# Performance work log

Hardware: AMD Instinct MI355X
Metric: run time of the kernel (lower is better)

## Reference

```python
import jax, jax.numpy as jnp
import numpy as np

B, N, C, T = 64, 1000, 64, 32


def setup_inputs() -> dict:
    key = jax.random.key(0)
    k = jax.random.split(key, 6)
    scale = 0.05
    return {
        "X": jax.random.normal(k[0], (B, N, C, T), dtype=jnp.float32),
        "U1": jax.random.normal(k[1], (N,), dtype=jnp.float32) * scale,
        "U2": jax.random.normal(k[2], (C, N), dtype=jnp.float32) * scale,
        "U3": jax.random.normal(k[3], (C,), dtype=jnp.float32) * scale,
        "be": jax.random.normal(k[4], (T, T), dtype=jnp.float32) * scale,
        "Ve": jax.random.normal(k[5], (T, T), dtype=jnp.float32) * scale,
    }


def reference(X, U1, U2, U3, be, Ve):
    # lhs: (X^T(0,3,2,1) @ U1) @ U2  -> (B, T, N)
    lhs = jnp.einsum('bnct,n->btc', X, U1) @ U2          # (B,T,N)
    # rhs: (X^T(0,3,1,2) @ U3)^T      -> (B, N, T)
    rhs = jnp.einsum('bnct,c->bnt', X, U3)               # (B,N,T)
    # scores: (B,T,T) + be
    scores = jnp.einsum('btn,bns->bts', lhs, rhs) + be   # (B,T,T)
    E = jnp.einsum('ts,bsu->btu', Ve, jax.nn.sigmoid(scores))  # Ve @ sigmoid
    E = jax.nn.softmax(E, axis=1)                        # softmax over dim=1
    # X_hat = X @ E (broadcast over node dim): (B,N,C,T) @ (B,1,T,T)
    X_hat = jnp.einsum('bnct,bts->bncs', X, E)
    return X_hat
```

## Files before the change

### kernel.cpp

```cpp
#include <hip/hip_runtime.h>
#include <math.h>

#define BB 64
#define NN 1000
#define CC 64
#define TT 32
#define NCH 40
#define NCHUNKS 25

typedef float floatx4 __attribute__((ext_vector_type(4)));

__global__ __launch_bounds__(256) void k_p1(const float* __restrict__ X,
                                            const float* __restrict__ U1,
                                            const float* __restrict__ U3,
                                            float* __restrict__ rhs,
                                            float* __restrict__ Apart) {
    int b  = blockIdx.x / NCHUNKS;
    int ch = blockIdx.x % NCHUNKS;
    int t  = threadIdx.x & 31;
    int nl = threadIdx.x >> 5;
    int n0 = ch * NCH;

    float accA[CC];
#pragma unroll
    for (int c = 0; c < CC; ++c) accA[c] = 0.f;

    for (int i = 0; i < NCH / 8; ++i) {
        int n = n0 + i * 8 + nl;
        const float* xp = X + ((size_t)(b * NN + n) * CC) * TT + t;
        float u1 = U1[n];
        float r = 0.f;
#pragma unroll
        for (int c = 0; c < CC; ++c) {
            float x = __builtin_nontemporal_load(&xp[c * TT]);
            r += U3[c] * x;
            accA[c] += u1 * x;
        }
        rhs[(size_t)(b * NN + n) * TT + t] = r;
    }

    __shared__ float buf[8][32][9];
    int t2 = threadIdx.x & 31;
    int j2 = threadIdx.x >> 5;
    for (int strip = 0; strip < 8; ++strip) {
        __syncthreads();
#pragma unroll
        for (int j = 0; j < 8; ++j) buf[nl][t][j] = accA[strip * 8 + j];
        __syncthreads();
        float v = 0.f;
#pragma unroll
        for (int k = 0; k < 8; ++k) v += buf[k][t2][j2];
        Apart[((size_t)(ch * BB + b) * TT + t2) * CC + strip * 8 + j2] = v;
    }
}

__global__ __launch_bounds__(256) void k_G(const float* __restrict__ rhs,
                                           const float* __restrict__ U2,
                                           float* __restrict__ G) {
    size_t idx = (size_t)blockIdx.x * blockDim.x + threadIdx.x;
    int s = (int)(idx & 31);
    int c = (int)((idx >> 5) & (CC - 1));
    int b = (int)(idx >> 11);
    const float* rp = rhs + (size_t)b * NN * TT + s;
    const float* up = U2 + (size_t)c * NN;
    float a0 = 0.f, a1 = 0.f, a2 = 0.f, a3 = 0.f;
#pragma unroll 2
    for (int n = 0; n < NN; n += 4) {
        a0 += up[n + 0] * rp[(size_t)(n + 0) * TT];
        a1 += up[n + 1] * rp[(size_t)(n + 1) * TT];
        a2 += up[n + 2] * rp[(size_t)(n + 2) * TT];
        a3 += up[n + 3] * rp[(size_t)(n + 3) * TT];
    }
    G[idx] = (a0 + a1) + (a2 + a3);
}

__global__ __launch_bounds__(1024) void k_E(const float* __restrict__ Apart,
                                            const float* __restrict__ G,
                                            const float* __restrict__ be,
                                            const float* __restrict__ Ve,
                                            float* __restrict__ E) {
    int b = blockIdx.x;
    int u = threadIdx.x & 31;
    int t = threadIdx.x >> 5;
    __shared__ float As[TT][CC + 1];
    __shared__ float sig[TT][TT];
    __shared__ float e0[TT][TT];

    float a0 = 0.f, a1 = 0.f;
    for (int ch = 0; ch < NCHUNKS; ++ch) {
        const float* ap = Apart + ((size_t)(ch * BB + b) * TT + t) * CC;
        a0 += ap[u];
        a1 += ap[u + 32];
    }
    As[t][u] = a0;
    As[t][u + 32] = a1;
    __syncthreads();

    const float* Gb = G + (size_t)b * CC * TT;
    float sc = be[t * TT + u];
#pragma unroll
    for (int c = 0; c < CC; ++c) {
        sc += As[t][c] * Gb[c * TT + u];
    }
    sig[t][u] = 1.f / (1.f + __expf(-sc));
    __syncthreads();

    float e = 0.f;
#pragma unroll
    for (int s = 0; s < TT; ++s) {
        e += Ve[t * TT + s] * sig[s][u];
    }
    e0[t][u] = e;
    __syncthreads();

    float m = -1e30f;
#pragma unroll
    for (int tt = 0; tt < TT; ++tt) m = fmaxf(m, e0[tt][u]);
    float mysig = __expf(e - m);
    float sum = 0.f;
#pragma unroll
    for (int tt = 0; tt < TT; ++tt) sum += __expf(e0[tt][u] - m);
    E[((size_t)b * TT + t) * TT + u] = mysig / sum;
}

__global__ __launch_bounds__(256) void k_xhat(const float* __restrict__ X,
                                              const float* __restrict__ E,
                                              float* __restrict__ Y) {
    const int blocks_per_b = (NN * CC) / 256;
    int b = blockIdx.x / blocks_per_b;
    int tid = threadIdx.x;
    size_t row = (size_t)blockIdx.x * 256 + tid;
    const float* xp = X + row * TT;
    float x[TT];
#pragma unroll
    for (int j = 0; j < TT / 4; ++j) {
        floatx4 v = *(const floatx4*)(xp + 4 * j);
        x[4 * j + 0] = v.x; x[4 * j + 1] = v.y;
        x[4 * j + 2] = v.z; x[4 * j + 3] = v.w;
    }
    const float* Eb = E + (size_t)b * TT * TT;
    float acc[TT];
#pragma unroll
    for (int s = 0; s < TT; ++s) acc[s] = 0.f;
#pragma unroll 4
    for (int t = 0; t < TT; ++t) {
        float xt = x[t];
#pragma unroll
        for (int s = 0; s < TT; ++s) {
            acc[s] += xt * Eb[t * TT + s];
        }
    }

    __shared__ floatx4 ly[256 * 8];
#pragma unroll
    for (int q = 0; q < 8; ++q) {
        floatx4 v = { acc[4 * q + 0], acc[4 * q + 1],
                      acc[4 * q + 2], acc[4 * q + 3] };
        ly[tid * 8 + (q ^ (tid & 7))] = v;
    }
    __syncthreads();

    floatx4* Yq = (floatx4*)Y;
    size_t qbase = (size_t)blockIdx.x * 2048;
#pragma unroll
    for (int k = 0; k < 8; ++k) {
        int g = k * 256 + tid;
        int lr = g >> 3;
        int q = g & 7;
        floatx4 v = ly[lr * 8 + (q ^ (lr & 7))];
        __builtin_nontemporal_store(v, &Yq[qbase + g]);
    }
}

extern "C" void kernel_launch(void* const* d_in, const int* in_sizes, int n_in,
                              void* d_out, int out_size, void* d_ws, size_t ws_size,
                              hipStream_t stream) {
    const float* X  = (const float*)d_in[0];
    const float* U1 = (const float*)d_in[1];
    const float* U2 = (const float*)d_in[2];
    const float* U3 = (const float*)d_in[3];
    const float* be = (const float*)d_in[4];
    const float* Ve = (const float*)d_in[5];
    float* Y = (float*)d_out;

    float* rhs   = (float*)d_ws;
    float* Apart = rhs + (size_t)BB * NN * TT;
    float* G     = Apart + (size_t)NCHUNKS * BB * TT * CC;
    float* E     = G + (size_t)BB * CC * TT;

    k_p1<<<BB * NCHUNKS, 256, 0, stream>>>(X, U1, U3, rhs, Apart);
    k_G<<<(BB * CC * TT) / 256, 256, 0, stream>>>(rhs, U2, G);
    k_E<<<BB, 1024, 0, stream>>>(Apart, G, be, Ve, E);
    k_xhat<<<BB * ((NN * CC) / 256), 256, 0, stream>>>(X, E, Y);
}
```

Before: 389.7 us.

## Split G reduction over node chunks and stage X loads through LDS

The k_G reduction over N is split into 8 chunks, giving eight times more threads, and the partial results are summed inside k_E, which now also stages G in shared memory. In k_xhat, X is loaded with coalesced nontemporal vector loads into swizzled LDS and then read row-wise, replacing strided per-thread row loads. The added costs are extra workspace traffic for the G partials and one more barrier in k_xhat.

```diff
diff --git a/kernel.cpp b/kernel.cpp
--- a/kernel.cpp
+++ b/kernel.cpp
@@ -7,6 +7,8 @@
 #define TT 32
 #define NCH 40
 #define NCHUNKS 25
+#define GSPLIT 8
+#define GCH 125
 
 typedef float floatx4 __attribute__((ext_vector_type(4)));
 
@@ -56,33 +58,39 @@
 
 __global__ __launch_bounds__(256) void k_G(const float* __restrict__ rhs,
                                            const float* __restrict__ U2,
-                                           float* __restrict__ G) {
-    size_t idx = (size_t)blockIdx.x * blockDim.x + threadIdx.x;
-    int s = (int)(idx & 31);
-    int c = (int)((idx >> 5) & (CC - 1));
-    int b = (int)(idx >> 11);
+                                           float* __restrict__ Gpart) {
+    size_t idx = (size_t)blockIdx.x * 256 + threadIdx.x;
+    int within = (int)(idx & (BB * CC * TT - 1));
+    int ch = (int)(idx >> 17);
+    int s = within & 31;
+    int c = (within >> 5) & (CC - 1);
+    int b = within >> 11;
     const float* rp = rhs + (size_t)b * NN * TT + s;
     const float* up = U2 + (size_t)c * NN;
-    float a0 = 0.f, a1 = 0.f, a2 = 0.f, a3 = 0.f;
-#pragma unroll 2
-    for (int n = 0; n < NN; n += 4) {
+    int n0 = ch * GCH;
+    float a0 = 0.f, a1 = 0.f, a2 = 0.f, a3 = 0.f, a4 = 0.f;
+    for (int i = 0; i < GCH; i += 5) {
+        int n = n0 + i;
         a0 += up[n + 0] * rp[(size_t)(n + 0) * TT];
         a1 += up[n + 1] * rp[(size_t)(n + 1) * TT];
         a2 += up[n + 2] * rp[(size_t)(n + 2) * TT];
         a3 += up[n + 3] * rp[(size_t)(n + 3) * TT];
-    }
-    G[idx] = (a0 + a1) + (a2 + a3);
+        a4 += up[n + 4] * rp[(size_t)(n + 4) * TT];
+    }
+    Gpart[idx] = ((a0 + a1) + (a2 + a3)) + a4;
 }
 
 __global__ __launch_bounds__(1024) void k_E(const float* __restrict__ Apart,
-                                            const float* __restrict__ G,
+                                            const float* __restrict__ Gpart,
                                             const float* __restrict__ be,
                                             const float* __restrict__ Ve,
                                             float* __restrict__ E) {
     int b = blockIdx.x;
-    int u = threadIdx.x & 31;
-    int t = threadIdx.x >> 5;
+    int tid = threadIdx.x;
+    int u = tid & 31;
+    int t = tid >> 5;
     __shared__ float As[TT][CC + 1];
+    __shared__ float Gs[CC * TT];
     __shared__ float sig[TT][TT];
     __shared__ float e0[TT][TT];
 
@@ -94,13 +102,22 @@
     }
     As[t][u] = a0;
     As[t][u + 32] = a1;
-    __syncthreads();
-
-    const float* Gb = G + (size_t)b * CC * TT;
+
+    float g0 = 0.f, g1 = 0.f;
+#pragma unroll
+    for (int ch = 0; ch < GSPLIT; ++ch) {
+        const float* gp = Gpart + (size_t)ch * (BB * CC * TT) + (size_t)b * CC * TT;
+        g0 += gp[tid];
+        g1 += gp[tid + 1024];
+    }
+    Gs[tid] = g0;
+    Gs[tid + 1024] = g1;
+    __syncthreads();
+
     float sc = be[t * TT + u];
 #pragma unroll
     for (int c = 0; c < CC; ++c) {
-        sc += As[t][c] * Gb[c * TT + u];
+        sc += As[t][c] * Gs[c * TT + u];
     }
     sig[t][u] = 1.f / (1.f + __expf(-sc));
     __syncthreads();
@@ -129,15 +146,28 @@
     const int blocks_per_b = (NN * CC) / 256;
     int b = blockIdx.x / blocks_per_b;
     int tid = threadIdx.x;
-    size_t row = (size_t)blockIdx.x * 256 + tid;
-    const float* xp = X + row * TT;
+    size_t qbase = (size_t)blockIdx.x * 2048;
+
+    __shared__ floatx4 ly[256 * 8];
+
+    const floatx4* Xq = (const floatx4*)X;
+#pragma unroll
+    for (int k = 0; k < 8; ++k) {
+        int g = k * 256 + tid;
+        int lr = g >> 3;
+        int q = g & 7;
+        ly[lr * 8 + (q ^ (lr & 7))] = __builtin_nontemporal_load(&Xq[qbase + g]);
+    }
+    __syncthreads();
+
     float x[TT];
 #pragma unroll
-    for (int j = 0; j < TT / 4; ++j) {
-        floatx4 v = *(const floatx4*)(xp + 4 * j);
+    for (int j = 0; j < 8; ++j) {
+        floatx4 v = ly[tid * 8 + (j ^ (tid & 7))];
         x[4 * j + 0] = v.x; x[4 * j + 1] = v.y;
         x[4 * j + 2] = v.z; x[4 * j + 3] = v.w;
     }
+
     const float* Eb = E + (size_t)b * TT * TT;
     float acc[TT];
 #pragma unroll
@@ -150,8 +180,8 @@
             acc[s] += xt * Eb[t * TT + s];
         }
     }
-
-    __shared__ floatx4 ly[256 * 8];
+    __syncthreads();
+
 #pragma unroll
     for (int q = 0; q < 8; ++q) {
         floatx4 v = { acc[4 * q + 0], acc[4 * q + 1],
@@ -161,7 +191,6 @@
     __syncthreads();
 
     floatx4* Yq = (floatx4*)Y;
-    size_t qbase = (size_t)blockIdx.x * 2048;
 #pragma unroll
     for (int k = 0; k < 8; ++k) {
         int g = k * 256 + tid;
@@ -185,11 +214,11 @@
 
     float* rhs   = (float*)d_ws;
     float* Apart = rhs + (size_t)BB * NN * TT;
-    float* G     = Apart + (size_t)NCHUNKS * BB * TT * CC;
-    float* E     = G + (size_t)BB * CC * TT;
+    float* Gpart = Apart + (size_t)NCHUNKS * BB * TT * CC;
+    float* E     = Gpart + (size_t)GSPLIT * BB * CC * TT;
 
     k_p1<<<BB * NCHUNKS, 256, 0, stream>>>(X, U1, U3, rhs, Apart);
-    k_G<<<(BB * CC * TT) / 256, 256, 0, stream>>>(rhs, U2, G);
-    k_E<<<BB, 1024, 0, stream>>>(Apart, G, be, Ve, E);
+    k_G<<<(GSPLIT * BB * CC * TT) / 256, 256, 0, stream>>>(rhs, U2, Gpart);
+    k_E<<<BB, 1024, 0, stream>>>(Apart, Gpart, be, Ve, E);
     k_xhat<<<BB * ((NN * CC) / 256), 256, 0, stream>>>(X, E, Y);
 }
```

Measured after the change: 406.4 us. +4.3%, slower.
